# Kernel optimization log

Measured on AMD Instinct MI355X. Metric: run time of the kernel, lower is better.

## Reference

```python
import jax, jax.numpy as jnp
import numpy as np

B, S, IN_DIM, H, NC = 4, 512, 32, 64, 3

def setup_inputs() -> dict:
    key = jax.random.key(0)
    ks = jax.random.split(key, 20)
    def lin(k, i, o):
        bound = 1.0 / np.sqrt(i)
        kw, kb = jax.random.split(k)
        W = jax.random.uniform(kw, (i, o), jnp.float32, -bound, bound)
        b = jax.random.uniform(kb, (o,), jnp.float32, -bound, bound)
        return W, b
    W1, b1 = lin(ks[0], IN_DIM, H)
    W2, b2 = lin(ks[1], H, H)
    We1, be1 = lin(ks[2], 2 * H, H)
    We2, be2 = lin(ks[3], H, H)
    Wd1, bd1 = lin(ks[4], 2 * H, H // 2)
    Wd2, bd2 = lin(ks[5], H // 2, 1)
    Wc1, bc1 = lin(ks[6], 2 * H, 32)
    Wc2, bc2 = lin(ks[7], 32, NC)
    x = jax.random.normal(ks[8], (B, S, IN_DIM), jnp.float32)
    return {"x": x, "W1": W1, "b1": b1, "W2": W2, "b2": b2,
            "We1": We1, "be1": be1, "We2": We2, "be2": be2,
            "Wd1": Wd1, "bd1": bd1, "Wd2": Wd2, "bd2": bd2,
            "Wc1": Wc1, "bc1": bc1, "Wc2": Wc2, "bc2": bc2}

def reference(x, W1, b1, W2, b2, We1, be1, We2, be2,
              Wd1, bd1, Wd2, bd2, Wc1, bc1, Wc2, bc2):
    b, s, _ = x.shape
    # node encoder: Linear -> ReLU -> Linear
    nodes = jax.nn.relu(x @ W1 + b1) @ W2 + b2          # [b,s,H]
    h = nodes.shape[-1]
    # all-pairs concat: pairs[b,i,j] = [nodes[b,i], nodes[b,j]]
    pi = jnp.broadcast_to(nodes[:, :, None, :], (b, s, s, h))
    pj = jnp.broadcast_to(nodes[:, None, :, :], (b, s, s, h))
    pairs = jnp.concatenate([pi, pj], axis=-1)          # [b,s,s,2H]
    # edge network
    raw_msgs = jax.nn.relu(pairs @ We1 + be1) @ We2 + be2   # [b,s,s,H]
    # demon gate
    keep = jax.nn.sigmoid(jax.nn.relu(pairs @ Wd1 + bd1) @ Wd2 + bd2)  # [b,s,s,1]
    active = (raw_msgs * keep).sum(axis=2)              # [b,s,H]
    trash = (raw_msgs * (1.0 - keep)).sum(axis=2)       # [b,s,H]
    main_emb = (nodes + active).mean(axis=1)            # [b,H]
    trash_emb = trash.mean(axis=1)                      # [b,H]
    feat = jnp.concatenate([main_emb, trash_emb], axis=-1)  # [b,2H]
    return jax.nn.relu(feat @ Wc1 + bc1) @ Wc2 + bc2    # [b,NC]
```

## Files before the change

kernel.cpp:

```cpp
#include <hip/hip_runtime.h>

#define BB 4
#define SS 512
#define IND 32
#define HH 64
#define NCC 3

#define IPB 4
#define NPB (BB * 256)
#define NNB 512

#define OFF_U    0
#define OFF_V    (OFF_U + BB*SS*HH)
#define OFF_P    (OFF_V + BB*SS*HH)
#define OFF_QT   (OFF_P + BB*SS*32)
#define OFF_SN   (OFF_QT + 32*BB*SS)
#define OFF_SA   (OFF_SN + NNB*HH)
#define OFF_SH   (OFF_SA + NPB*HH)
#define OFF_SKP  (OFF_SH + NPB*HH)

__device__ __forceinline__ float rl(float v, int l) {
    return __uint_as_float(__builtin_amdgcn_readlane(__float_as_uint(v), l));
}

__global__ __launch_bounds__(256) void k_nodes(
    const float* __restrict__ x,  const float* __restrict__ W1, const float* __restrict__ b1,
    const float* __restrict__ W2, const float* __restrict__ b2,
    const float* __restrict__ We1,const float* __restrict__ be1,
    const float* __restrict__ Wd1,const float* __restrict__ bd1,
    float* __restrict__ ws)
{
    float* U = ws + OFF_U;  float* V4 = ws + OFF_V;
    float* P = ws + OFF_P;  float* Qt4 = ws + OFF_QT;
    float* SN = ws + OFF_SN;
    __shared__ float sn_lds[4][64];
    const int tid = threadIdx.x, wave = tid >> 6, lane = tid & 63;
    const int L = ((blockIdx.x & 7) << 6) | (blockIdx.x >> 3);
    const int node = L * 4 + wave;

    float xv = (lane < IND) ? x[node * IND + lane] : 0.0f;
    float h1 = b1[lane];
    #pragma unroll
    for (int k = 0; k < IND; k++)
        h1 = fmaf(__shfl(xv, k, 64), W1[k * HH + lane], h1);
    h1 = fmaxf(h1, 0.0f);

    float nd = b2[lane];
    #pragma unroll 16
    for (int k = 0; k < HH; k++)
        nd = fmaf(__shfl(h1, k, 64), W2[k * HH + lane], nd);

    float uv = be1[lane];
    float vv = 0.0f;
    float pq = (lane < 32) ? bd1[lane] : 0.0f;
    const float* WdCol = (lane < 32) ? (Wd1 + lane) : (Wd1 + HH * 32 + (lane - 32));
    #pragma unroll 16
    for (int k = 0; k < HH; k++) {
        float s = __shfl(nd, k, 64);
        uv = fmaf(s, We1[k * HH + lane], uv);
        vv = fmaf(s, We1[(HH + k) * HH + lane], vv);
        pq = fmaf(s, WdCol[k * 32], pq);
    }
    U[node * HH + lane] = uv;
    V4[(L * 64 + lane) * 4 + wave] = vv;
    if (lane < 32) {
        P[node * 32 + lane] = pq;
    } else {
        int k = lane - 32;
        Qt4[((k >> 2) * (BB * SS) + node) * 4 + (k & 3)] = pq;
    }

    sn_lds[wave][lane] = nd;
    __syncthreads();
    if (tid < 64)
        SN[L * 64 + tid] = (sn_lds[0][tid] + sn_lds[1][tid]) + (sn_lds[2][tid] + sn_lds[3][tid]);
}

__global__ __launch_bounds__(256, 4) void k_pairs(
    const float* __restrict__ wd2, const float* __restrict__ bd2,
    float* __restrict__ ws)
{
    const float*  U   = ws + OFF_U;
    const float4* V4  = (const float4*)(ws + OFF_V);
    const float*  P   = ws + OFF_P;
    const float4* Qt4 = (const float4*)(ws + OFF_QT);
    float* SA = ws + OFF_SA;  float* SHo = ws + OFF_SH;  float* SKp = ws + OFF_SKP;

    __shared__ float redA[4][64], redH[4][64], redK[4];

    const int tid = threadIdx.x, wave = tid >> 6, lane = tid & 63;
    const int d   = blockIdx.x;
    const int xcd = d & 7;
    const int b   = xcd >> 1;
    const int jc  = xcd & 1;
    const int ic  = d >> 3;
    const int i0  = ic * IPB;
    const int lidx = (b << 8) | (ic << 1) | jc;
    const int jbase = b * SS + jc * 256 + wave * 64;

    const float4* Qp = Qt4 + jbase + lane;
    const float4* Vp = V4 + (jbase >> 2) * 64 + lane;
    float4 q[8], v[16];
    #pragma unroll
    for (int kg = 0; kg < 8; kg++) q[kg] = Qp[kg * (BB * SS)];
    #pragma unroll
    for (int jq = 0; jq < 8; jq++) v[jq] = Vp[jq * 64];

    const float u0 = U[(b * SS + i0 + 0) * HH + lane];
    const float u1 = U[(b * SS + i0 + 1) * HH + lane];
    const float u2 = U[(b * SS + i0 + 2) * HH + lane];
    const float u3 = U[(b * SS + i0 + 3) * HH + lane];
    const float pk0 = P[(b * SS + i0 + 0) * 32 + (lane & 31)];
    const float pk1 = P[(b * SS + i0 + 1) * 32 + (lane & 31)];
    const float pk2 = P[(b * SS + i0 + 2) * 32 + (lane & 31)];
    const float pk3 = P[(b * SS + i0 + 3) * 32 + (lane & 31)];
    const float wv  = wd2[lane & 31];
    const float bd2v = bd2[0];

    __builtin_amdgcn_sched_barrier(0);

    float a0 = bd2v, a1 = bd2v, a2 = bd2v, a3 = bd2v;
    #pragma unroll
    for (int kg = 0; kg < 8; kg++) {
        #pragma unroll
        for (int t = 0; t < 4; t++) {
            const int k = kg * 4 + t;
            float qv = (t == 0) ? q[kg].x : (t == 1) ? q[kg].y : (t == 2) ? q[kg].z : q[kg].w;
            float w  = rl(wv, k);
            a0 = fmaf(w, fmaxf(rl(pk0, k) + qv, 0.0f), a0);
            a1 = fmaf(w, fmaxf(rl(pk1, k) + qv, 0.0f), a1);
            a2 = fmaf(w, fmaxf(rl(pk2, k) + qv, 0.0f), a2);
            a3 = fmaf(w, fmaxf(rl(pk3, k) + qv, 0.0f), a3);
        }
    }
    float g0 = 1.0f / (1.0f + __expf(-a0));
    float g1 = 1.0f / (1.0f + __expf(-a1));
    float g2 = 1.0f / (1.0f + __expf(-a2));
    float g3 = 1.0f / (1.0f + __expf(-a3));
    float sk = (g0 + g1) + (g2 + g3);

    #pragma unroll
    for (int jq = 8; jq < 16; jq++) v[jq] = Vp[jq * 64];

    float sa = 0.0f, sh = 0.0f;
    #pragma unroll
    for (int jq = 0; jq < 16; jq++) {
        #pragma unroll
        for (int t = 0; t < 4; t++) {
            const int joff = jq * 4 + t;
            float vv = (t == 0) ? v[jq].x : (t == 1) ? v[jq].y : (t == 2) ? v[jq].z : v[jq].w;
            float h0 = fmaxf(u0 + vv, 0.0f);
            float h1 = fmaxf(u1 + vv, 0.0f);
            float h2 = fmaxf(u2 + vv, 0.0f);
            float h3 = fmaxf(u3 + vv, 0.0f);
            sh += (h0 + h1) + (h2 + h3);
            sa = fmaf(rl(g0, joff), h0, sa);
            sa = fmaf(rl(g1, joff), h1, sa);
            sa = fmaf(rl(g2, joff), h2, sa);
            sa = fmaf(rl(g3, joff), h3, sa);
        }
    }

    redA[wave][lane] = sa;
    redH[wave][lane] = sh;
    #pragma unroll
    for (int off = 32; off; off >>= 1) sk += __shfl_xor(sk, off, 64);
    if (lane == 0) redK[wave] = sk;
    __syncthreads();

    if (tid < 64) {
        SA[lidx * 64 + tid]  = (redA[0][tid] + redA[1][tid]) + (redA[2][tid] + redA[3][tid]);
        SHo[lidx * 64 + tid] = (redH[0][tid] + redH[1][tid]) + (redH[2][tid] + redH[3][tid]);
        if (tid == 0)
            SKp[lidx * 16] = (redK[0] + redK[1]) + (redK[2] + redK[3]);
    }
}

__global__ __launch_bounds__(256) void k_final(
    const float* __restrict__ We2, const float* __restrict__ be2,
    const float* __restrict__ Wc1, const float* __restrict__ bc1,
    const float* __restrict__ Wc2, const float* __restrict__ bc2,
    const float* __restrict__ ws, float* __restrict__ out)
{
    const float4* SN4 = (const float4*)(ws + OFF_SN);
    const float4* SA4 = (const float4*)(ws + OFF_SA);
    const float4* SH4 = (const float4*)(ws + OFF_SH);
    const float*  SKp = ws + OFF_SKP;
    __shared__ float4 r4[3][16][16];
    __shared__ float redS[256], saL[64], shL[64];
    __shared__ float featL[128], c1L[32];
    const int tid = threadIdx.x, wave = tid >> 6, lane = tid & 63;
    const int grp = tid >> 4, l16 = tid & 15;
    const int b = blockIdx.x;

    float4 sn4 = make_float4(0.f, 0.f, 0.f, 0.f);
    float4 sa4 = sn4, sh4 = sn4;
    #pragma unroll
    for (int r = 0; r < 8; r++) {
        float4 t = SN4[(b * 128 + r * 16 + grp) * 16 + l16];
        sn4.x += t.x; sn4.y += t.y; sn4.z += t.z; sn4.w += t.w;
    }
    #pragma unroll
    for (int r = 0; r < 16; r++) {
        float4 t = SA4[(b * 256 + r * 16 + grp) * 16 + l16];
        float4 u = SH4[(b * 256 + r * 16 + grp) * 16 + l16];
        sa4.x += t.x; sa4.y += t.y; sa4.z += t.z; sa4.w += t.w;
        sh4.x += u.x; sh4.y += u.y; sh4.z += u.z; sh4.w += u.w;
    }
    r4[0][grp][l16] = sn4;  r4[1][grp][l16] = sa4;  r4[2][grp][l16] = sh4;
    redS[tid] = SKp[(b * 256 + tid) * 16];
    __syncthreads();

    if (wave == 0) {
        const int li = lane >> 2, comp = lane & 3;
        float snT = 0.f, saF = 0.f, shF = 0.f;
        #pragma unroll
        for (int g = 0; g < 16; g++) {
            snT += ((const float*)&r4[0][g][li])[comp];
            saF += ((const float*)&r4[1][g][li])[comp];
            shF += ((const float*)&r4[2][g][li])[comp];
        }
        float skp = (redS[lane] + redS[64 + lane]) + (redS[128 + lane] + redS[192 + lane]);
        #pragma unroll
        for (int off = 32; off; off >>= 1) skp += __shfl_xor(skp, off, 64);
        saL[lane] = saF;  shL[lane] = shF;

        float as = skp * be2[lane];
        float ts = (262144.0f - skp) * be2[lane];
        #pragma unroll 8
        for (int k = 0; k < HH; k++) {
            float w = We2[k * HH + lane];
            float sak = saL[k];
            as = fmaf(sak, w, as);
            ts = fmaf(shL[k] - sak, w, ts);
        }
        featL[lane]      = (snT + as) * (1.0f / 512.0f);
        featL[64 + lane] = ts * (1.0f / 512.0f);
    }
    __syncthreads();

    if (tid < 32) {
        float c1 = bc1[tid];
        #pragma unroll 8
        for (int k = 0; k < 128; k++)
            c1 = fmaf(featL[k], Wc1[k * 32 + tid], c1);
        c1L[tid] = fmaxf(c1, 0.0f);
    }
    __syncthreads();
    if (tid < NCC) {
        float o = bc2[tid];
        #pragma unroll
        for (int k = 0; k < 32; k++)
            o = fmaf(c1L[k], Wc2[k * NCC + tid], o);
        out[b * NCC + tid] = o;
    }
}

extern "C" void kernel_launch(void* const* d_in, const int* in_sizes, int n_in,
                              void* d_out, int out_size, void* d_ws, size_t ws_size,
                              hipStream_t stream) {
    const float* x   = (const float*)d_in[0];
    const float* W1  = (const float*)d_in[1];
    const float* b1  = (const float*)d_in[2];
    const float* W2  = (const float*)d_in[3];
    const float* b2  = (const float*)d_in[4];
    const float* We1 = (const float*)d_in[5];
    const float* be1 = (const float*)d_in[6];
    const float* We2 = (const float*)d_in[7];
    const float* be2 = (const float*)d_in[8];
    const float* Wd1 = (const float*)d_in[9];
    const float* bd1 = (const float*)d_in[10];
    const float* wd2 = (const float*)d_in[11];
    const float* bd2 = (const float*)d_in[12];
    const float* Wc1 = (const float*)d_in[13];
    const float* bc1 = (const float*)d_in[14];
    const float* Wc2 = (const float*)d_in[15];
    const float* bc2 = (const float*)d_in[16];
    float* ws  = (float*)d_ws;
    float* out = (float*)d_out;

    k_nodes<<<dim3(NNB), dim3(256), 0, stream>>>(x, W1, b1, W2, b2, We1, be1, Wd1, bd1, ws);
    k_pairs<<<dim3(NPB), dim3(256), 0, stream>>>(wd2, bd2, ws);
    k_final<<<dim3(BB), dim3(256), 0, stream>>>(We2, be2, Wc1, bc1, Wc2, bc2, ws, out);
}
```

Measured before the change: 36.24 us.

## Make k_pairs blocks loop over eight i-chunks, reusing loaded Q/V tiles

Each k_pairs block now iterates over eight consecutive i-groups instead of one, keeping its per-wave q and v register tiles resident across iterations. The next group's U and P rows are prefetched inside the loop. The grid shrinks from 1024 to 128 blocks and launch bounds drop to one block per SM. The aim is to cut repeated global loads of the j-side data and per-block launch overhead. In exchange it adds an extra __syncthreads per iteration and leaves far fewer blocks to hide latency across the GPU's CUs.

After: 53.19 us. 1.47x slower.

```diff
diff --git a/kernel.cpp b/kernel.cpp
--- a/kernel.cpp
+++ b/kernel.cpp
@@ -7,7 +7,7 @@
 #define NCC 3
 
 #define IPB 4
-#define NPB (BB * 256)
+#define NPB 128
 #define NNB 512
 
 #define OFF_U    0
@@ -16,8 +16,8 @@
 #define OFF_QT   (OFF_P + BB*SS*32)
 #define OFF_SN   (OFF_QT + 32*BB*SS)
 #define OFF_SA   (OFF_SN + NNB*HH)
-#define OFF_SH   (OFF_SA + NPB*HH)
-#define OFF_SKP  (OFF_SH + NPB*HH)
+#define OFF_SH   (OFF_SA + 1024*HH)
+#define OFF_SKP  (OFF_SH + 1024*HH)
 
 __device__ __forceinline__ float rl(float v, int l) {
     return __uint_as_float(__builtin_amdgcn_readlane(__float_as_uint(v), l));
@@ -76,7 +76,7 @@
         SN[L * 64 + tid] = (sn_lds[0][tid] + sn_lds[1][tid]) + (sn_lds[2][tid] + sn_lds[3][tid]);
 }
 
-__global__ __launch_bounds__(256, 4) void k_pairs(
+__global__ __launch_bounds__(256, 1) void k_pairs(
     const float* __restrict__ wd2, const float* __restrict__ bd2,
     float* __restrict__ ws)
 {
@@ -93,9 +93,7 @@
     const int xcd = d & 7;
     const int b   = xcd >> 1;
     const int jc  = xcd & 1;
-    const int ic  = d >> 3;
-    const int i0  = ic * IPB;
-    const int lidx = (b << 8) | (ic << 1) | jc;
+    const int grp = d >> 3;
     const int jbase = b * SS + jc * 256 + wave * 64;
 
     const float4* Qp = Qt4 + jbase + lane;
@@ -104,75 +102,92 @@
     #pragma unroll
     for (int kg = 0; kg < 8; kg++) q[kg] = Qp[kg * (BB * SS)];
     #pragma unroll
-    for (int jq = 0; jq < 8; jq++) v[jq] = Vp[jq * 64];
-
-    const float u0 = U[(b * SS + i0 + 0) * HH + lane];
-    const float u1 = U[(b * SS + i0 + 1) * HH + lane];
-    const float u2 = U[(b * SS + i0 + 2) * HH + lane];
-    const float u3 = U[(b * SS + i0 + 3) * HH + lane];
-    const float pk0 = P[(b * SS + i0 + 0) * 32 + (lane & 31)];
-    const float pk1 = P[(b * SS + i0 + 1) * 32 + (lane & 31)];
-    const float pk2 = P[(b * SS + i0 + 2) * 32 + (lane & 31)];
-    const float pk3 = P[(b * SS + i0 + 3) * 32 + (lane & 31)];
+    for (int jq = 0; jq < 16; jq++) v[jq] = Vp[jq * 64];
     const float wv  = wd2[lane & 31];
     const float bd2v = bd2[0];
 
-    __builtin_amdgcn_sched_barrier(0);
-
-    float a0 = bd2v, a1 = bd2v, a2 = bd2v, a3 = bd2v;
-    #pragma unroll
-    for (int kg = 0; kg < 8; kg++) {
-        #pragma unroll
-        for (int t = 0; t < 4; t++) {
-            const int k = kg * 4 + t;
-            float qv = (t == 0) ? q[kg].x : (t == 1) ? q[kg].y : (t == 2) ? q[kg].z : q[kg].w;
-            float w  = rl(wv, k);
-            a0 = fmaf(w, fmaxf(rl(pk0, k) + qv, 0.0f), a0);
-            a1 = fmaf(w, fmaxf(rl(pk1, k) + qv, 0.0f), a1);
-            a2 = fmaf(w, fmaxf(rl(pk2, k) + qv, 0.0f), a2);
-            a3 = fmaf(w, fmaxf(rl(pk3, k) + qv, 0.0f), a3);
-        }
-    }
-    float g0 = 1.0f / (1.0f + __expf(-a0));
-    float g1 = 1.0f / (1.0f + __expf(-a1));
-    float g2 = 1.0f / (1.0f + __expf(-a2));
-    float g3 = 1.0f / (1.0f + __expf(-a3));
-    float sk = (g0 + g1) + (g2 + g3);
-
-    #pragma unroll
-    for (int jq = 8; jq < 16; jq++) v[jq] = Vp[jq * 64];
-
-    float sa = 0.0f, sh = 0.0f;
-    #pragma unroll
-    for (int jq = 0; jq < 16; jq++) {
-        #pragma unroll
-        for (int t = 0; t < 4; t++) {
-            const int joff = jq * 4 + t;
-            float vv = (t == 0) ? v[jq].x : (t == 1) ? v[jq].y : (t == 2) ? v[jq].z : v[jq].w;
-            float h0 = fmaxf(u0 + vv, 0.0f);
-            float h1 = fmaxf(u1 + vv, 0.0f);
-            float h2 = fmaxf(u2 + vv, 0.0f);
-            float h3 = fmaxf(u3 + vv, 0.0f);
-            sh += (h0 + h1) + (h2 + h3);
-            sa = fmaf(rl(g0, joff), h0, sa);
-            sa = fmaf(rl(g1, joff), h1, sa);
-            sa = fmaf(rl(g2, joff), h2, sa);
-            sa = fmaf(rl(g3, joff), h3, sa);
-        }
-    }
-
-    redA[wave][lane] = sa;
-    redH[wave][lane] = sh;
-    #pragma unroll
-    for (int off = 32; off; off >>= 1) sk += __shfl_xor(sk, off, 64);
-    if (lane == 0) redK[wave] = sk;
-    __syncthreads();
-
-    if (tid < 64) {
-        SA[lidx * 64 + tid]  = (redA[0][tid] + redA[1][tid]) + (redA[2][tid] + redA[3][tid]);
-        SHo[lidx * 64 + tid] = (redH[0][tid] + redH[1][tid]) + (redH[2][tid] + redH[3][tid]);
-        if (tid == 0)
-            SKp[lidx * 16] = (redK[0] + redK[1]) + (redK[2] + redK[3]);
+    const int i00 = grp * 8 * IPB;
+    float u0 = U[(b * SS + i00 + 0) * HH + lane];
+    float u1 = U[(b * SS + i00 + 1) * HH + lane];
+    float u2 = U[(b * SS + i00 + 2) * HH + lane];
+    float u3 = U[(b * SS + i00 + 3) * HH + lane];
+    float pk0 = P[(b * SS + i00 + 0) * 32 + (lane & 31)];
+    float pk1 = P[(b * SS + i00 + 1) * 32 + (lane & 31)];
+    float pk2 = P[(b * SS + i00 + 2) * 32 + (lane & 31)];
+    float pk3 = P[(b * SS + i00 + 3) * 32 + (lane & 31)];
+
+    #pragma unroll 1
+    for (int t = 0; t < 8; t++) {
+        const int ic = grp * 8 + t;
+        const int lidx = (b << 8) | (ic << 1) | jc;
+
+        float a0 = bd2v, a1 = bd2v, a2 = bd2v, a3 = bd2v;
+        #pragma unroll
+        for (int kg = 0; kg < 8; kg++) {
+            #pragma unroll
+            for (int tt = 0; tt < 4; tt++) {
+                const int k = kg * 4 + tt;
+                float qv = (tt == 0) ? q[kg].x : (tt == 1) ? q[kg].y : (tt == 2) ? q[kg].z : q[kg].w;
+                float w  = rl(wv, k);
+                a0 = fmaf(w, fmaxf(rl(pk0, k) + qv, 0.0f), a0);
+                a1 = fmaf(w, fmaxf(rl(pk1, k) + qv, 0.0f), a1);
+                a2 = fmaf(w, fmaxf(rl(pk2, k) + qv, 0.0f), a2);
+                a3 = fmaf(w, fmaxf(rl(pk3, k) + qv, 0.0f), a3);
+            }
+        }
+        float g0 = 1.0f / (1.0f + __expf(-a0));
+        float g1 = 1.0f / (1.0f + __expf(-a1));
+        float g2 = 1.0f / (1.0f + __expf(-a2));
+        float g3 = 1.0f / (1.0f + __expf(-a3));
+        float sk = (g0 + g1) + (g2 + g3);
+
+        const int tn = (t + 1) & 7;
+        const int in0 = (grp * 8 + tn) * IPB;
+        float nu0 = U[(b * SS + in0 + 0) * HH + lane];
+        float nu1 = U[(b * SS + in0 + 1) * HH + lane];
+        float nu2 = U[(b * SS + in0 + 2) * HH + lane];
+        float nu3 = U[(b * SS + in0 + 3) * HH + lane];
+        float np0 = P[(b * SS + in0 + 0) * 32 + (lane & 31)];
+        float np1 = P[(b * SS + in0 + 1) * 32 + (lane & 31)];
+        float np2 = P[(b * SS + in0 + 2) * 32 + (lane & 31)];
+        float np3 = P[(b * SS + in0 + 3) * 32 + (lane & 31)];
+
+        float sa = 0.0f, sh = 0.0f;
+        #pragma unroll
+        for (int jq = 0; jq < 16; jq++) {
+            #pragma unroll
+            for (int tt = 0; tt < 4; tt++) {
+                const int joff = jq * 4 + tt;
+                float vv = (tt == 0) ? v[jq].x : (tt == 1) ? v[jq].y : (tt == 2) ? v[jq].z : v[jq].w;
+                float h0 = fmaxf(u0 + vv, 0.0f);
+                float h1 = fmaxf(u1 + vv, 0.0f);
+                float h2 = fmaxf(u2 + vv, 0.0f);
+                float h3 = fmaxf(u3 + vv, 0.0f);
+                sh += (h0 + h1) + (h2 + h3);
+                sa = fmaf(rl(g0, joff), h0, sa);
+                sa = fmaf(rl(g1, joff), h1, sa);
+                sa = fmaf(rl(g2, joff), h2, sa);
+                sa = fmaf(rl(g3, joff), h3, sa);
+            }
+        }
+
+        redA[wave][lane] = sa;
+        redH[wave][lane] = sh;
+        #pragma unroll
+        for (int off = 32; off; off >>= 1) sk += __shfl_xor(sk, off, 64);
+        if (lane == 0) redK[wave] = sk;
+        __syncthreads();
+
+        if (tid < 64) {
+            SA[lidx * 64 + tid]  = (redA[0][tid] + redA[1][tid]) + (redA[2][tid] + redA[3][tid]);
+            SHo[lidx * 64 + tid] = (redH[0][tid] + redH[1][tid]) + (redH[2][tid] + redH[3][tid]);
+            if (tid == 0)
+                SKp[lidx * 16] = (redK[0] + redK[1]) + (redK[2] + redK[3]);
+        }
+        __syncthreads();
+
+        u0 = nu0; u1 = nu1; u2 = nu2; u3 = nu3;
+        pk0 = np0; pk1 = np1; pk2 = np2; pk3 = np3;
     }
 }
 
```
